# Performance work log

Hardware: AMD Instinct MI355X
Metric: run time of the kernel (lower is better)

Reference implementation:

```python
import jax, jax.numpy as jnp
import numpy as np

PATCH = 8
C1 = 1e-4
C2 = 1e-3
EPS = 1e-3
ALPHA = 0.4
WEIGHTS = (1.0, 0.01, 1.0)


def charbonnier(x):
    return (x * x + EPS * EPS) ** ALPHA


def resize_bilinear_ac(img, H2, W2):
    # bilinear resize with align_corners=True (matches F.interpolate)
    B, C, H, W = img.shape
    fy = jnp.arange(H2, dtype=img.dtype) * ((H - 1) / max(H2 - 1, 1))
    fx = jnp.arange(W2, dtype=img.dtype) * ((W - 1) / max(W2 - 1, 1))
    y0 = jnp.clip(jnp.floor(fy).astype(jnp.int32), 0, H - 2)
    x0 = jnp.clip(jnp.floor(fx).astype(jnp.int32), 0, W - 2)
    wy = (fy - y0)[None, None, :, None]
    wx = (fx - x0)[None, None, None, :]
    rows = img[:, :, y0, :] * (1 - wy) + img[:, :, y0 + 1, :] * wy  # [B,C,H2,W]
    out = rows[:, :, :, x0] * (1 - wx) + rows[:, :, :, x0 + 1] * wx  # [B,C,H2,W2]
    return out


def bilinear_warp(img, flow):
    # backward warp: sample img at (x + u, y + v), bilinear, border clamp
    B, C, H, W = img.shape
    gx = jnp.arange(W, dtype=img.dtype)[None, None, :] + flow[:, 0]  # [B,H,W]
    gy = jnp.arange(H, dtype=img.dtype)[None, :, None] + flow[:, 1]  # [B,H,W]
    x0f = jnp.floor(gx)
    y0f = jnp.floor(gy)
    wx = (gx - x0f)[:, None]  # [B,1,H,W]
    wy = (gy - y0f)[:, None]
    x0 = jnp.clip(x0f.astype(jnp.int32), 0, W - 1)
    x1 = jnp.clip(x0 + 1, 0, W - 1)
    y0 = jnp.clip(y0f.astype(jnp.int32), 0, H - 1)
    y1 = jnp.clip(y0 + 1, 0, H - 1)
    imgf = img.reshape(B, C, H * W)

    def gather(yi, xi):
        idx = (yi * W + xi).reshape(B, 1, H * W)
        g = jnp.take_along_axis(imgf, jnp.broadcast_to(idx, (B, C, H * W)), axis=2)
        return g.reshape(B, C, H, W)

    v00 = gather(y0, x0)
    v01 = gather(y0, x1)
    v10 = gather(y1, x0)
    v11 = gather(y1, x1)
    top = v00 * (1 - wx) + v01 * wx
    bot = v10 * (1 - wx) + v11 * wx
    return top * (1 - wy) + bot * wy


def torch_gradient(x, axis):
    # torch.gradient: central diff interior, one-sided at edges, spacing 1
    n = x.shape[axis]
    sl = lambda a, b: jax.lax.slice_in_dim(x, a, b, axis=axis)
    first = sl(1, 2) - sl(0, 1)
    interior = (sl(2, n) - sl(0, n - 2)) * 0.5
    last = sl(n - 1, n) - sl(n - 2, n - 1)
    return jnp.concatenate([first, interior, last], axis=axis)


def ssim_score(I1, I2):
    # faithful to SSIMLoss: stats pooled over ALL non-overlapping patches per
    # (batch, channel), i.e. over the region cropped to multiples of patch.
    B, C, H, W = I1.shape
    p = min(PATCH, H)
    PH, PW = H // p, W // p
    x = I1[:, :, :PH * p, :PW * p].reshape(B, C, -1)
    y = I2[:, :, :PH * p, :PW * p].reshape(B, C, -1)
    N = x.shape[-1]
    mu1 = x.mean(-1)
    mu2 = y.mean(-1)
    d1 = x - mu1[..., None]
    d2 = y - mu2[..., None]
    var1 = (d1 * d1).sum(-1) / (N - 1)  # torch .var() is unbiased
    var2 = (d2 * d2).sum(-1) / (N - 1)
    s12 = (d1 * d2).mean(-1)
    num = (2 * mu1 * mu2 + C1) * (2 * s12 + C2)
    den = (mu1 ** 2 + mu2 ** 2 + C1) * (var1 + var2 + C2)
    return num / den  # [B, C]


def setup_inputs() -> dict:
    key = jax.random.key(0)
    k1, k2 = jax.random.split(key)
    images = jax.random.uniform(k1, (16, 33, 256, 256), dtype=jnp.float32)
    flows = jax.random.normal(k2, (16, 20, 128, 128), dtype=jnp.float32)
    return {"images": images, "flows": flows}


def reference(images, flows):
    B, Cf, FH, FW = flows.shape
    n_flows = Cf // 2  # 10 frame pairs
    imgs = resize_bilinear_ac(images, FH, FW)  # [B,33,FH,FW]
    src = imgs[:, 3:].reshape(B * n_flows, 3, FH, FW)
    fl = flows.reshape(B * n_flows, 2, FH, FW)
    warped = bilinear_warp(src, fl).reshape(B, n_flows * 3, FH, FW)
    ref = imgs[:, : n_flows * 3]

    similarity_loss = ssim_score(ref, warped).mean()

    flow_x = flows[:, 0::2]
    flow_y = flows[:, 1::2]
    smooth = (charbonnier(torch_gradient(flow_x, 1))
              + charbonnier(torch_gradient(flow_x, 2))
              + charbonnier(torch_gradient(flow_y, 1))
              + charbonnier(torch_gradient(flow_y, 2))).mean()

    pixel_loss = charbonnier(ref - warped).mean()

    return WEIGHTS[0] * pixel_loss + WEIGHTS[1] * smooth + WEIGHTS[2] * similarity_loss
```

## Files before the change

kernel.cpp:

```cpp
#include <hip/hip_runtime.h>

#define IH 256
#define IW 256
#define FH 128
#define FW 128
#define NB 16
#define ICH 33
#define NF 10
#define NC 30
#define PL (FH * FW)
#define ACC_FLOATS 3848
#define RES_OFF 4096
#define RES_CNT (NB * ICH * PL)
#define WS_NEED ((size_t)(RES_OFF + RES_CNT) * 4)

__device__ __forceinline__ float charb(float g) {
    float t = fmaf(g, g, 1e-6f);
    return __builtin_amdgcn_exp2f(0.4f * __builtin_amdgcn_logf(t));
}

__global__ void __launch_bounds__(256) resize_kernel(const float* __restrict__ images,
                                                     float* __restrict__ resized,
                                                     float* __restrict__ acc)
{
    if (blockIdx.x == 0) {
        for (int i = threadIdx.x; i < ACC_FLOATS; i += 256) acc[i] = 0.f;
    }
    __shared__ float rows[4][256];
    const float s = (float)(255.0 / 127.0);
    int plane = blockIdx.x >> 6;
    int j = blockIdx.x & 63;
    int h0 = 2 * j;
    int y0a = (int)((float)h0 * s);       if (y0a > IH - 2) y0a = IH - 2;
    int y0b = (int)((float)(h0 + 1) * s); if (y0b > IH - 2) y0b = IH - 2;
    int rowidx[4] = { y0a, y0a + 1, y0b, y0b + 1 };
    const float* pin = images + (size_t)plane * (IH * IW);
    int r = threadIdx.x >> 6;
    int l = threadIdx.x & 63;
    const float4* srcv = (const float4*)(pin + rowidx[r] * IW);
    ((float4*)rows[r])[l] = srcv[l];
    __syncthreads();
    int lr = threadIdx.x >> 7;
    int w = threadIdx.x & 127;
    int h = h0 + lr;
    float fy = (float)h * s;
    int y0 = lr ? y0b : y0a;
    float wy = fy - (float)y0;
    float fx = (float)w * s;
    int x0 = (int)fx; if (x0 > IW - 2) x0 = IW - 2;
    float wx = fx - (float)x0;
    float v00 = rows[2 * lr][x0],     v01 = rows[2 * lr][x0 + 1];
    float v10 = rows[2 * lr + 1][x0], v11 = rows[2 * lr + 1][x0 + 1];
    float r0 = v00 * (1.f - wy) + v10 * wy;
    float r1 = v01 * (1.f - wy) + v11 * wy;
    resized[(size_t)plane * PL + h * FW + w] = r0 * (1.f - wx) + r1 * wx;
}

__device__ __forceinline__ float warp_sample(const float* __restrict__ src_plane,
                                             float gx, float gy) {
    float x0f = floorf(gx), y0f = floorf(gy);
    float wx = gx - x0f, wy = gy - y0f;
    int x0 = (int)x0f; x0 = min(max(x0, 0), FW - 1);
    int y0 = (int)y0f; y0 = min(max(y0, 0), FH - 1);
    int x1 = min(x0 + 1, FW - 1);
    int y1 = min(y0 + 1, FH - 1);
    const float* r0p = src_plane + y0 * FW;
    const float* r1p = src_plane + y1 * FW;
    float v00 = r0p[x0], v01 = r0p[x1];
    float v10 = r1p[x0], v11 = r1p[x1];
    float top = v00 * (1.f - wx) + v01 * wx;
    float bot = v10 * (1.f - wx) + v11 * wx;
    return top * (1.f - wy) + bot * wy;
}

#define SPLIT 4
#define LOSS_BLOCKS (NB * NC * SPLIT)
#define SMOOTH_BLOCKS 1280
#define PIX_PER_BLOCK (PL / SPLIT)
__global__ void __launch_bounds__(256) fat_kernel(const float* __restrict__ resized,
                                                  const float* __restrict__ flows,
                                                  float* __restrict__ acc_bc,
                                                  float* __restrict__ acc_g)
{
    if (blockIdx.x < LOSS_BLOCKS) {
        int bc = blockIdx.x / SPLIT;
        int part = blockIdx.x % SPLIT;
        int b = bc / NC;
        int c = bc % NC;
        int f = c / 3;
        const float* ref_plane = resized + (size_t)(b * ICH + c) * PL;
        const float* src_plane = resized + (size_t)(b * ICH + 3 + c) * PL;
        const float* fx_plane  = flows + (size_t)(b * 2 * NF + 2 * f) * PL;
        const float* fy_plane  = fx_plane + PL;

        float s_ref = 0.f, s_w = 0.f, s_r2 = 0.f, s_w2 = 0.f, s_rw = 0.f, s_pix = 0.f;
        int base2 = part * (PIX_PER_BLOCK / 2);
        for (int i = threadIdx.x; i < PIX_PER_BLOCK / 2; i += 256) {
            int pix2 = base2 + i;
            int pix = pix2 * 2;
            int h = pix >> 7;
            int w = pix & (FW - 1);
            float2 ref2 = ((const float2*)ref_plane)[pix2];
            float2 fx2  = ((const float2*)fx_plane)[pix2];
            float2 fy2  = ((const float2*)fy_plane)[pix2];

            float wv0 = warp_sample(src_plane, (float)w + fx2.x,       (float)h + fy2.x);
            float wv1 = warp_sample(src_plane, (float)(w + 1) + fx2.y, (float)h + fy2.y);

            s_ref += ref2.x + ref2.y;
            s_w   += wv0 + wv1;
            s_r2  += ref2.x * ref2.x + ref2.y * ref2.y;
            s_w2  += wv0 * wv0 + wv1 * wv1;
            s_rw  += ref2.x * wv0 + ref2.y * wv1;
            s_pix += charb(ref2.x - wv0) + charb(ref2.y - wv1);
        }
        for (int off = 32; off > 0; off >>= 1) {
            s_ref += __shfl_down(s_ref, off, 64);
            s_w   += __shfl_down(s_w, off, 64);
            s_r2  += __shfl_down(s_r2, off, 64);
            s_w2  += __shfl_down(s_w2, off, 64);
            s_rw  += __shfl_down(s_rw, off, 64);
            s_pix += __shfl_down(s_pix, off, 64);
        }
        __shared__ float sh[4][6];
        int wave = threadIdx.x >> 6;
        if ((threadIdx.x & 63) == 0) {
            sh[wave][0] = s_ref; sh[wave][1] = s_w; sh[wave][2] = s_r2;
            sh[wave][3] = s_w2;  sh[wave][4] = s_rw; sh[wave][5] = s_pix;
        }
        __syncthreads();
        if (threadIdx.x == 0) {
            float t0 = 0, t1 = 0, t2 = 0, t3 = 0, t4 = 0, t5 = 0;
            for (int v = 0; v < 4; v++) {
                t0 += sh[v][0]; t1 += sh[v][1]; t2 += sh[v][2];
                t3 += sh[v][3]; t4 += sh[v][4]; t5 += sh[v][5];
            }
            float* a = acc_bc + bc * 8;
            atomicAdd(a + 0, t0);
            atomicAdd(a + 1, t1);
            atomicAdd(a + 2, t2);
            atomicAdd(a + 3, t3);
            atomicAdd(a + 4, t4);
            atomicAdd(acc_g + 0, t5);
        }
    } else {
        const int total = NB * NF * PL;
        float s = 0.f;
        for (int i = (blockIdx.x - LOSS_BLOCKS) * 256 + threadIdx.x; i < total;
             i += SMOOTH_BLOCKS * 256) {
            int w = i & (FW - 1);
            int h = (i >> 7) & (FH - 1);
            int f = (i >> 14) % NF;
            int b = i / (NF * PL);
            int pix = h * FW + w;
            const float* xp = flows + (size_t)(b * 2 * NF + 2 * f) * PL;
            const float* yp = xp + PL;

            float g1x, g1y;
            if (f == 0)           { g1x = xp[2 * PL + pix] - xp[pix];
                                    g1y = yp[2 * PL + pix] - yp[pix]; }
            else if (f == NF - 1) { g1x = xp[pix] - xp[pix - 2 * PL];
                                    g1y = yp[pix] - yp[pix - 2 * PL]; }
            else                  { g1x = 0.5f * (xp[2 * PL + pix] - xp[pix - 2 * PL]);
                                    g1y = 0.5f * (yp[2 * PL + pix] - yp[pix - 2 * PL]); }

            float g2x, g2y;
            if (h == 0)           { g2x = xp[pix + FW] - xp[pix];
                                    g2y = yp[pix + FW] - yp[pix]; }
            else if (h == FH - 1) { g2x = xp[pix] - xp[pix - FW];
                                    g2y = yp[pix] - yp[pix - FW]; }
            else                  { g2x = 0.5f * (xp[pix + FW] - xp[pix - FW]);
                                    g2y = 0.5f * (yp[pix + FW] - yp[pix - FW]); }

            s += charb(g1x) + charb(g2x) + charb(g1y) + charb(g2y);
        }
        for (int off = 32; off > 0; off >>= 1) s += __shfl_down(s, off, 64);
        __shared__ float shs[4];
        int wave = threadIdx.x >> 6;
        if ((threadIdx.x & 63) == 0) shs[wave] = s;
        __syncthreads();
        if (threadIdx.x == 0)
            atomicAdd(acc_g + 2, shs[0] + shs[1] + shs[2] + shs[3]);
    }
}

__global__ void __launch_bounds__(512) finalize(const float* __restrict__ acc_bc,
                                                const float* __restrict__ acc_g,
                                                float* __restrict__ out)
{
    __shared__ float sh[512];
    int tid = threadIdx.x;
    float ssim = 0.f;
    if (tid < NB * NC) {
        const float* a = acc_bc + tid * 8;
        const float N = (float)PL;
        float mu1 = a[0] / N, mu2 = a[1] / N;
        float var1 = (a[2] - a[0] * mu1) / (N - 1.f);
        float var2 = (a[3] - a[1] * mu2) / (N - 1.f);
        float s12 = a[4] / N - mu1 * mu2;
        float num = (2.f * mu1 * mu2 + 1e-4f) * (2.f * s12 + 1e-3f);
        float den = (mu1 * mu1 + mu2 * mu2 + 1e-4f) * (var1 + var2 + 1e-3f);
        ssim = num / den;
    }
    sh[tid] = ssim;
    __syncthreads();
    for (int off = 256; off > 0; off >>= 1) {
        if (tid < off) sh[tid] += sh[tid + off];
        __syncthreads();
    }
    if (tid == 0) {
        float pix    = acc_g[0] / (float)(NB * NC * PL);
        float smooth = acc_g[2] / (float)(NB * NF * PL);
        float sim    = sh[0] / (float)(NB * NC);
        out[0] = pix + 0.01f * smooth + sim;
    }
}

__device__ __forceinline__ float resized_at(const float* __restrict__ plane, int Y, int X) {
    const float s = (float)(255.0 / 127.0);
    float fy = (float)Y * s;
    float fx = (float)X * s;
    int y0 = (int)fy; y0 = y0 > IH - 2 ? IH - 2 : y0;
    int x0 = (int)fx; x0 = x0 > IW - 2 ? IW - 2 : x0;
    float wy = fy - (float)y0;
    float wx = fx - (float)x0;
    const float* p0 = plane + y0 * IW + x0;
    float v00 = p0[0], v01 = p0[1];
    float v10 = p0[IW], v11 = p0[IW + 1];
    float r0 = v00 * (1.f - wy) + v10 * wy;
    float r1 = v01 * (1.f - wy) + v11 * wy;
    return r0 * (1.f - wx) + r1 * wx;
}

__global__ void __launch_bounds__(256) loss_main_fb(const float* __restrict__ images,
                                                    const float* __restrict__ flows,
                                                    float* __restrict__ acc_bc,
                                                    float* __restrict__ acc_g)
{
    int bc = blockIdx.x / 8;
    int part = blockIdx.x % 8;
    int b = bc / NC;
    int c = bc % NC;
    int f = c / 3;
    const float* ref_plane = images + (size_t)(b * ICH + c) * (IH * IW);
    const float* src_plane = images + (size_t)(b * ICH + 3 + c) * (IH * IW);
    const float* fx_plane  = flows + (size_t)(b * 2 * NF + 2 * f) * PL;
    const float* fy_plane  = fx_plane + PL;

    float s_ref = 0.f, s_w = 0.f, s_r2 = 0.f, s_w2 = 0.f, s_rw = 0.f, s_pix = 0.f;
    int base = part * (PL / 8);
    for (int i = threadIdx.x; i < PL / 8; i += 256) {
        int pix = base + i;
        int h = pix >> 7;
        int w = pix & (FW - 1);
        float ref = resized_at(ref_plane, h, w);
        float fxv = fx_plane[pix];
        float fyv = fy_plane[pix];
        float gx = (float)w + fxv;
        float gy = (float)h + fyv;
        float x0f = floorf(gx), y0f = floorf(gy);
        float wx = gx - x0f, wy = gy - y0f;
        int x0 = (int)x0f; x0 = min(max(x0, 0), FW - 1);
        int y0 = (int)y0f; y0 = min(max(y0, 0), FH - 1);
        int x1 = min(x0 + 1, FW - 1);
        int y1 = min(y0 + 1, FH - 1);
        float v00 = resized_at(src_plane, y0, x0);
        float v01 = resized_at(src_plane, y0, x1);
        float v10 = resized_at(src_plane, y1, x0);
        float v11 = resized_at(src_plane, y1, x1);
        float top = v00 * (1.f - wx) + v01 * wx;
        float bot = v10 * (1.f - wx) + v11 * wx;
        float wv = top * (1.f - wy) + bot * wy;
        s_ref += ref; s_w += wv;
        s_r2 += ref * ref; s_w2 += wv * wv; s_rw += ref * wv;
        s_pix += charb(ref - wv);
    }
    for (int off = 32; off > 0; off >>= 1) {
        s_ref += __shfl_down(s_ref, off, 64);
        s_w   += __shfl_down(s_w, off, 64);
        s_r2  += __shfl_down(s_r2, off, 64);
        s_w2  += __shfl_down(s_w2, off, 64);
        s_rw  += __shfl_down(s_rw, off, 64);
        s_pix += __shfl_down(s_pix, off, 64);
    }
    if ((threadIdx.x & 63) == 0) {
        float* a = acc_bc + bc * 8;
        atomicAdd(a + 0, s_ref);
        atomicAdd(a + 1, s_w);
        atomicAdd(a + 2, s_r2);
        atomicAdd(a + 3, s_w2);
        atomicAdd(a + 4, s_rw);
        atomicAdd(acc_g + 0, s_pix);
    }
}

__global__ void __launch_bounds__(256) smooth_fb(const float* __restrict__ flows,
                                                 float* __restrict__ acc_g)
{
    const int total = NB * NF * PL;
    float s = 0.f;
    for (int i = blockIdx.x * 256 + threadIdx.x; i < total; i += 1280 * 256) {
        int w = i & (FW - 1);
        int h = (i >> 7) & (FH - 1);
        int f = (i >> 14) % NF;
        int b = i / (NF * PL);
        int pix = h * FW + w;
        const float* xp = flows + (size_t)(b * 2 * NF + 2 * f) * PL;
        const float* yp = xp + PL;
        float g1x, g1y;
        if (f == 0)           { g1x = xp[2 * PL + pix] - xp[pix];
                                g1y = yp[2 * PL + pix] - yp[pix]; }
        else if (f == NF - 1) { g1x = xp[pix] - xp[pix - 2 * PL];
                                g1y = yp[pix] - yp[pix - 2 * PL]; }
        else                  { g1x = 0.5f * (xp[2 * PL + pix] - xp[pix - 2 * PL]);
                                g1y = 0.5f * (yp[2 * PL + pix] - yp[pix - 2 * PL]); }
        float g2x, g2y;
        if (h == 0)           { g2x = xp[pix + FW] - xp[pix];
                                g2y = yp[pix + FW] - yp[pix]; }
        else if (h == FH - 1) { g2x = xp[pix] - xp[pix - FW];
                                g2y = yp[pix] - yp[pix - FW]; }
        else                  { g2x = 0.5f * (xp[pix + FW] - xp[pix - FW]);
                                g2y = 0.5f * (yp[pix + FW] - yp[pix - FW]); }
        s += charb(g1x) + charb(g2x) + charb(g1y) + charb(g2y);
    }
    for (int off = 32; off > 0; off >>= 1) s += __shfl_down(s, off, 64);
    __shared__ float sh[4];
    int wave = threadIdx.x >> 6;
    if ((threadIdx.x & 63) == 0) sh[wave] = s;
    __syncthreads();
    if (threadIdx.x == 0)
        atomicAdd(acc_g + 2, sh[0] + sh[1] + sh[2] + sh[3]);
}

extern "C" void kernel_launch(void* const* d_in, const int* in_sizes, int n_in,
                              void* d_out, int out_size, void* d_ws, size_t ws_size,
                              hipStream_t stream) {
    const float* images = (const float*)d_in[0];
    const float* flows  = (const float*)d_in[1];
    float* acc_bc  = (float*)d_ws;
    float* acc_g   = acc_bc + NB * NC * 8;
    float* resized = (float*)d_ws + RES_OFF;
    if (ws_size >= WS_NEED) {
        resize_kernel<<<NB * ICH * (FH / 2), 256, 0, stream>>>(images, resized, acc_bc);
        fat_kernel<<<LOSS_BLOCKS + SMOOTH_BLOCKS, 256, 0, stream>>>(resized, flows,
                                                                    acc_bc, acc_g);
    } else {
        (void)hipMemsetAsync(d_ws, 0, ACC_FLOATS * sizeof(float), stream);
        loss_main_fb<<<NB * NC * 8, 256, 0, stream>>>(images, flows, acc_bc, acc_g);
        smooth_fb<<<1280, 256, 0, stream>>>(flows, acc_g);
    }
    finalize<<<1, 512, 0, stream>>>(acc_bc, acc_g, (float*)d_out);
}
```

Before: 261.6 us.

## Move smoothness term into resize kernel and fuse finalize via last-block counter

The flow smoothness reduction moves from the loss kernel into the resize kernel, so it runs alongside the resize and writes per-block partials instead of using atomics. The finalize kernel is removed: the last loss block, found with an atomic counter and a threadfence, computes SSIM and the final sum. The loss kernel now processes four pixels per thread with float4 loads, and its block index is remapped so each batch image's blocks land on one XCD for L2 locality. This saves a kernel launch and the tail of the loss kernel, but adds the threadfence and counter ordering and has the last block re-read the accumulators with atomics.

Result: slower. 285.4 us (+9.1%).

```diff
diff --git a/kernel.cpp b/kernel.cpp
--- a/kernel.cpp
+++ b/kernel.cpp
@@ -9,8 +9,10 @@
 #define NF 10
 #define NC 30
 #define PL (FH * FW)
-#define ACC_FLOATS 3848
-#define RES_OFF 4096
+#define ACC_ZERO 3856
+#define SMOOTH_BLK 1280
+#define RES_BLK (NB * ICH * 64)
+#define RES_OFF 8192
 #define RES_CNT (NB * ICH * PL)
 #define WS_NEED ((size_t)(RES_OFF + RES_CNT) * 4)
 
@@ -19,25 +21,71 @@
     return __builtin_amdgcn_exp2f(0.4f * __builtin_amdgcn_logf(t));
 }
 
-__global__ void __launch_bounds__(256) resize_kernel(const float* __restrict__ images,
-                                                     float* __restrict__ resized,
-                                                     float* __restrict__ acc)
+__global__ void __launch_bounds__(256) k1_smooth_resize(const float* __restrict__ images,
+                                                        const float* __restrict__ flows,
+                                                        float* __restrict__ ws)
 {
+    float* acc         = ws;
+    float* smooth_part = ws + ACC_ZERO;
+    float* resized     = ws + RES_OFF;
+
     if (blockIdx.x == 0) {
-        for (int i = threadIdx.x; i < ACC_FLOATS; i += 256) acc[i] = 0.f;
-    }
+        for (int i = threadIdx.x; i < ACC_ZERO; i += 256) acc[i] = 0.f;
+    }
+
+    if (blockIdx.x < SMOOTH_BLK) {
+        const int total = NB * NF * PL;
+        float s = 0.f;
+        for (int i = blockIdx.x * 256 + threadIdx.x; i < total; i += SMOOTH_BLK * 256) {
+            int w = i & (FW - 1);
+            int h = (i >> 7) & (FH - 1);
+            int f = (i >> 14) % NF;
+            int b = i / (NF * PL);
+            int pix = h * FW + w;
+            const float* xp = flows + (size_t)(b * 2 * NF + 2 * f) * PL;
+            const float* yp = xp + PL;
+
+            float g1x, g1y;
+            if (f == 0)           { g1x = xp[2 * PL + pix] - xp[pix];
+                                    g1y = yp[2 * PL + pix] - yp[pix]; }
+            else if (f == NF - 1) { g1x = xp[pix] - xp[pix - 2 * PL];
+                                    g1y = yp[pix] - yp[pix - 2 * PL]; }
+            else                  { g1x = 0.5f * (xp[2 * PL + pix] - xp[pix - 2 * PL]);
+                                    g1y = 0.5f * (yp[2 * PL + pix] - yp[pix - 2 * PL]); }
+
+            float g2x, g2y;
+            if (h == 0)           { g2x = xp[pix + FW] - xp[pix];
+                                    g2y = yp[pix + FW] - yp[pix]; }
+            else if (h == FH - 1) { g2x = xp[pix] - xp[pix - FW];
+                                    g2y = yp[pix] - yp[pix - FW]; }
+            else                  { g2x = 0.5f * (xp[pix + FW] - xp[pix - FW]);
+                                    g2y = 0.5f * (yp[pix + FW] - yp[pix - FW]); }
+
+            s += charb(g1x) + charb(g2x) + charb(g1y) + charb(g2y);
+        }
+        for (int off = 32; off > 0; off >>= 1) s += __shfl_down(s, off, 64);
+        __shared__ float shs[4];
+        int wave = threadIdx.x >> 6;
+        if ((threadIdx.x & 63) == 0) shs[wave] = s;
+        __syncthreads();
+        if (threadIdx.x == 0)
+            smooth_part[blockIdx.x] = shs[0] + shs[1] + shs[2] + shs[3];
+        return;
+    }
+
+    int rb = blockIdx.x - SMOOTH_BLK;
     __shared__ float rows[4][256];
     const float s = (float)(255.0 / 127.0);
-    int plane = blockIdx.x >> 6;
-    int j = blockIdx.x & 63;
+    int plane = rb >> 6;
+    int j = rb & 63;
     int h0 = 2 * j;
     int y0a = (int)((float)h0 * s);       if (y0a > IH - 2) y0a = IH - 2;
     int y0b = (int)((float)(h0 + 1) * s); if (y0b > IH - 2) y0b = IH - 2;
-    int rowidx[4] = { y0a, y0a + 1, y0b, y0b + 1 };
     const float* pin = images + (size_t)plane * (IH * IW);
     int r = threadIdx.x >> 6;
     int l = threadIdx.x & 63;
-    const float4* srcv = (const float4*)(pin + rowidx[r] * IW);
+    int yr = (r < 2 ? y0a : y0b) + (r & 1);
+    const float4* srcv = (const float4*)(pin + yr * IW);
     ((float4*)rows[r])[l] = srcv[l];
     __syncthreads();
     int lr = threadIdx.x >> 7;
@@ -75,144 +123,128 @@
 
 #define SPLIT 4
 #define LOSS_BLOCKS (NB * NC * SPLIT)
-#define SMOOTH_BLOCKS 1280
 #define PIX_PER_BLOCK (PL / SPLIT)
-__global__ void __launch_bounds__(256) fat_kernel(const float* __restrict__ resized,
-                                                  const float* __restrict__ flows,
-                                                  float* __restrict__ acc_bc,
-                                                  float* __restrict__ acc_g)
+__global__ void __launch_bounds__(256) k2_loss_final(const float* __restrict__ flows,
+                                                     float* __restrict__ ws,
+                                                     float* __restrict__ out)
 {
-    if (blockIdx.x < LOSS_BLOCKS) {
-        int bc = blockIdx.x / SPLIT;
-        int part = blockIdx.x % SPLIT;
-        int b = bc / NC;
-        int c = bc % NC;
-        int f = c / 3;
-        const float* ref_plane = resized + (size_t)(b * ICH + c) * PL;
-        const float* src_plane = resized + (size_t)(b * ICH + 3 + c) * PL;
-        const float* fx_plane  = flows + (size_t)(b * 2 * NF + 2 * f) * PL;
-        const float* fy_plane  = fx_plane + PL;
-
-        float s_ref = 0.f, s_w = 0.f, s_r2 = 0.f, s_w2 = 0.f, s_rw = 0.f, s_pix = 0.f;
-        int base2 = part * (PIX_PER_BLOCK / 2);
-        for (int i = threadIdx.x; i < PIX_PER_BLOCK / 2; i += 256) {
-            int pix2 = base2 + i;
-            int pix = pix2 * 2;
-            int h = pix >> 7;
-            int w = pix & (FW - 1);
-            float2 ref2 = ((const float2*)ref_plane)[pix2];
-            float2 fx2  = ((const float2*)fx_plane)[pix2];
-            float2 fy2  = ((const float2*)fy_plane)[pix2];
-
-            float wv0 = warp_sample(src_plane, (float)w + fx2.x,       (float)h + fy2.x);
-            float wv1 = warp_sample(src_plane, (float)(w + 1) + fx2.y, (float)h + fy2.y);
-
-            s_ref += ref2.x + ref2.y;
-            s_w   += wv0 + wv1;
-            s_r2  += ref2.x * ref2.x + ref2.y * ref2.y;
-            s_w2  += wv0 * wv0 + wv1 * wv1;
-            s_rw  += ref2.x * wv0 + ref2.y * wv1;
-            s_pix += charb(ref2.x - wv0) + charb(ref2.y - wv1);
+    float* acc_bc      = ws;
+    float* acc_g       = ws + 3840;
+    unsigned* counter  = (unsigned*)(ws + 3848);
+    const float* smooth_part = ws + ACC_ZERO;
+    const float* resized     = ws + RES_OFF;
+
+    int xcd  = blockIdx.x & 7;
+    int slot = blockIdx.x >> 3;
+    int hi   = (slot >= 120) ? 1 : 0;
+    int b    = xcd + 8 * hi;
+    int j    = slot - 120 * hi;
+    int c    = j >> 2;
+    int part = j & 3;
+    int bc   = b * NC + c;
+    int f    = c / 3;
+
+    const float* ref_plane = resized + (size_t)(b * ICH + c) * PL;
+    const float* src_plane = resized + (size_t)(b * ICH + 3 + c) * PL;
+    const float* fx_plane  = flows + (size_t)(b * 2 * NF + 2 * f) * PL;
+    const float* fy_plane  = fx_plane + PL;
+
+    float s_ref = 0.f, s_w = 0.f, s_r2 = 0.f, s_w2 = 0.f, s_rw = 0.f, s_pix = 0.f;
+    int base4 = part * (PIX_PER_BLOCK / 4);
+    for (int i = threadIdx.x; i < PIX_PER_BLOCK / 4; i += 256) {
+        int p4 = base4 + i;
+        int pix = p4 * 4;
+        int h = pix >> 7;
+        int w = pix & (FW - 1);
+        float4 r4 = ((const float4*)ref_plane)[p4];
+        float4 fx4 = ((const float4*)fx_plane)[p4];
+        float4 fy4 = ((const float4*)fy_plane)[p4];
+        float fh = (float)h, fw0 = (float)w;
+
+        float wv0 = warp_sample(src_plane, fw0 + fx4.x,       fh + fy4.x);
+        float wv1 = warp_sample(src_plane, fw0 + 1.f + fx4.y, fh + fy4.y);
+        float wv2 = warp_sample(src_plane, fw0 + 2.f + fx4.z, fh + fy4.z);
+        float wv3 = warp_sample(src_plane, fw0 + 3.f + fx4.w, fh + fy4.w);
+
+        s_ref += (r4.x + r4.y) + (r4.z + r4.w);
+        s_w   += (wv0 + wv1) + (wv2 + wv3);
+        s_r2  += r4.x * r4.x + r4.y * r4.y + r4.z * r4.z + r4.w * r4.w;
+        s_w2  += wv0 * wv0 + wv1 * wv1 + wv2 * wv2 + wv3 * wv3;
+        s_rw  += r4.x * wv0 + r4.y * wv1 + r4.z * wv2 + r4.w * wv3;
+        s_pix += charb(r4.x - wv0) + charb(r4.y - wv1)
+               + charb(r4.z - wv2) + charb(r4.w - wv3);
+    }
+    for (int off = 32; off > 0; off >>= 1) {
+        s_ref += __shfl_down(s_ref, off, 64);
+        s_w   += __shfl_down(s_w, off, 64);
+        s_r2  += __shfl_down(s_r2, off, 64);
+        s_w2  += __shfl_down(s_w2, off, 64);
+        s_rw  += __shfl_down(s_rw, off, 64);
+        s_pix += __shfl_down(s_pix, off, 64);
+    }
+    __shared__ float sh[4][6];
+    __shared__ int last_flag;
+    int wave = threadIdx.x >> 6;
+    if ((threadIdx.x & 63) == 0) {
+        sh[wave][0] = s_ref; sh[wave][1] = s_w; sh[wave][2] = s_r2;
+        sh[wave][3] = s_w2;  sh[wave][4] = s_rw; sh[wave][5] = s_pix;
+    }
+    __syncthreads();
+    if (threadIdx.x == 0) {
+        float t0 = 0, t1 = 0, t2 = 0, t3 = 0, t4 = 0, t5 = 0;
+        for (int v = 0; v < 4; v++) {
+            t0 += sh[v][0]; t1 += sh[v][1]; t2 += sh[v][2];
+            t3 += sh[v][3]; t4 += sh[v][4]; t5 += sh[v][5];
         }
-        for (int off = 32; off > 0; off >>= 1) {
-            s_ref += __shfl_down(s_ref, off, 64);
-            s_w   += __shfl_down(s_w, off, 64);
-            s_r2  += __shfl_down(s_r2, off, 64);
-            s_w2  += __shfl_down(s_w2, off, 64);
-            s_rw  += __shfl_down(s_rw, off, 64);
-            s_pix += __shfl_down(s_pix, off, 64);
-        }
-        __shared__ float sh[4][6];
-        int wave = threadIdx.x >> 6;
-        if ((threadIdx.x & 63) == 0) {
-            sh[wave][0] = s_ref; sh[wave][1] = s_w; sh[wave][2] = s_r2;
-            sh[wave][3] = s_w2;  sh[wave][4] = s_rw; sh[wave][5] = s_pix;
-        }
-        __syncthreads();
-        if (threadIdx.x == 0) {
-            float t0 = 0, t1 = 0, t2 = 0, t3 = 0, t4 = 0, t5 = 0;
-            for (int v = 0; v < 4; v++) {
-                t0 += sh[v][0]; t1 += sh[v][1]; t2 += sh[v][2];
-                t3 += sh[v][3]; t4 += sh[v][4]; t5 += sh[v][5];
-            }
-            float* a = acc_bc + bc * 8;
-            atomicAdd(a + 0, t0);
-            atomicAdd(a + 1, t1);
-            atomicAdd(a + 2, t2);
-            atomicAdd(a + 3, t3);
-            atomicAdd(a + 4, t4);
-            atomicAdd(acc_g + 0, t5);
-        }
-    } else {
-        const int total = NB * NF * PL;
-        float s = 0.f;
-        for (int i = (blockIdx.x - LOSS_BLOCKS) * 256 + threadIdx.x; i < total;
-             i += SMOOTH_BLOCKS * 256) {
-            int w = i & (FW - 1);
-            int h = (i >> 7) & (FH - 1);
-            int f = (i >> 14) % NF;
-            int b = i / (NF * PL);
-            int pix = h * FW + w;
-            const float* xp = flows + (size_t)(b * 2 * NF + 2 * f) * PL;
-            const float* yp = xp + PL;
-
-            float g1x, g1y;
-            if (f == 0)           { g1x = xp[2 * PL + pix] - xp[pix];
-                                    g1y = yp[2 * PL + pix] - yp[pix]; }
-            else if (f == NF - 1) { g1x = xp[pix] - xp[pix - 2 * PL];
-                                    g1y = yp[pix] - yp[pix - 2 * PL]; }
-            else                  { g1x = 0.5f * (xp[2 * PL + pix] - xp[pix - 2 * PL]);
-                                    g1y = 0.5f * (yp[2 * PL + pix] - yp[pix - 2 * PL]); }
-
-            float g2x, g2y;
-            if (h == 0)           { g2x = xp[pix + FW] - xp[pix];
-                                    g2y = yp[pix + FW] - yp[pix]; }
-            else if (h == FH - 1) { g2x = xp[pix] - xp[pix - FW];
-                                    g2y = yp[pix] - yp[pix - FW]; }
-            else                  { g2x = 0.5f * (xp[pix + FW] - xp[pix - FW]);
-                                    g2y = 0.5f * (yp[pix + FW] - yp[pix - FW]); }
-
-            s += charb(g1x) + charb(g2x) + charb(g1y) + charb(g2y);
-        }
-        for (int off = 32; off > 0; off >>= 1) s += __shfl_down(s, off, 64);
-        __shared__ float shs[4];
-        int wave = threadIdx.x >> 6;
-        if ((threadIdx.x & 63) == 0) shs[wave] = s;
-        __syncthreads();
-        if (threadIdx.x == 0)
-            atomicAdd(acc_g + 2, shs[0] + shs[1] + shs[2] + shs[3]);
-    }
-}
-
-__global__ void __launch_bounds__(512) finalize(const float* __restrict__ acc_bc,
-                                                const float* __restrict__ acc_g,
-                                                float* __restrict__ out)
-{
-    __shared__ float sh[512];
-    int tid = threadIdx.x;
-    float ssim = 0.f;
-    if (tid < NB * NC) {
-        const float* a = acc_bc + tid * 8;
+        float* a = acc_bc + bc * 8;
+        atomicAdd(a + 0, t0);
+        atomicAdd(a + 1, t1);
+        atomicAdd(a + 2, t2);
+        atomicAdd(a + 3, t3);
+        atomicAdd(a + 4, t4);
+        atomicAdd(acc_g + 0, t5);
+        __threadfence();
+        unsigned old = atomicAdd(counter, 1u);
+        last_flag = (old == LOSS_BLOCKS - 1) ? 1 : 0;
+    }
+    __syncthreads();
+    if (!last_flag) return;
+
+    float ssim_s = 0.f;
+    for (int e = threadIdx.x; e < NB * NC; e += 256) {
+        float* a = acc_bc + e * 8;
+        float t0 = atomicAdd(a + 0, 0.f);
+        float t1 = atomicAdd(a + 1, 0.f);
+        float t2 = atomicAdd(a + 2, 0.f);
+        float t3 = atomicAdd(a + 3, 0.f);
+        float t4 = atomicAdd(a + 4, 0.f);
         const float N = (float)PL;
-        float mu1 = a[0] / N, mu2 = a[1] / N;
-        float var1 = (a[2] - a[0] * mu1) / (N - 1.f);
-        float var2 = (a[3] - a[1] * mu2) / (N - 1.f);
-        float s12 = a[4] / N - mu1 * mu2;
+        float mu1 = t0 / N, mu2 = t1 / N;
+        float var1 = (t2 - t0 * mu1) / (N - 1.f);
+        float var2 = (t3 - t1 * mu2) / (N - 1.f);
+        float s12 = t4 / N - mu1 * mu2;
         float num = (2.f * mu1 * mu2 + 1e-4f) * (2.f * s12 + 1e-3f);
         float den = (mu1 * mu1 + mu2 * mu2 + 1e-4f) * (var1 + var2 + 1e-3f);
-        ssim = num / den;
-    }
-    sh[tid] = ssim;
-    __syncthreads();
-    for (int off = 256; off > 0; off >>= 1) {
-        if (tid < off) sh[tid] += sh[tid + off];
-        __syncthreads();
-    }
-    if (tid == 0) {
-        float pix    = acc_g[0] / (float)(NB * NC * PL);
-        float smooth = acc_g[2] / (float)(NB * NF * PL);
-        float sim    = sh[0] / (float)(NB * NC);
-        out[0] = pix + 0.01f * smooth + sim;
+        ssim_s += num / den;
+    }
+    float smooth_s = 0.f;
+    for (int i = threadIdx.x; i < SMOOTH_BLK; i += 256)
+        smooth_s += smooth_part[i];
+
+    for (int off = 32; off > 0; off >>= 1) {
+        ssim_s   += __shfl_down(ssim_s, off, 64);
+        smooth_s += __shfl_down(smooth_s, off, 64);
+    }
+    __shared__ float fs[4][2];
+    if ((threadIdx.x & 63) == 0) { fs[wave][0] = ssim_s; fs[wave][1] = smooth_s; }
+    __syncthreads();
+    if (threadIdx.x == 0) {
+        float ssim_t = fs[0][0] + fs[1][0] + fs[2][0] + fs[3][0];
+        float smo_t  = fs[0][1] + fs[1][1] + fs[2][1] + fs[3][1];
+        float pix_t  = atomicAdd(acc_g + 0, 0.f);
+        out[0] = pix_t / (float)(NB * NC * PL)
+               + 0.01f * (smo_t / (float)(NB * NF * PL))
+               + ssim_t / (float)(NB * NC);
     }
 }
 
@@ -246,7 +278,6 @@
     const float* src_plane = images + (size_t)(b * ICH + 3 + c) * (IH * IW);
     const float* fx_plane  = flows + (size_t)(b * 2 * NF + 2 * f) * PL;
     const float* fy_plane  = fx_plane + PL;
-
     float s_ref = 0.f, s_w = 0.f, s_r2 = 0.f, s_w2 = 0.f, s_rw = 0.f, s_pix = 0.f;
     int base = part * (PL / 8);
     for (int i = threadIdx.x; i < PL / 8; i += 256) {
@@ -254,10 +285,8 @@
         int h = pix >> 7;
         int w = pix & (FW - 1);
         float ref = resized_at(ref_plane, h, w);
-        float fxv = fx_plane[pix];
-        float fyv = fy_plane[pix];
-        float gx = (float)w + fxv;
-        float gy = (float)h + fyv;
+        float gx = (float)w + fx_plane[pix];
+        float gy = (float)h + fy_plane[pix];
         float x0f = floorf(gx), y0f = floorf(gy);
         float wx = gx - x0f, wy = gy - y0f;
         int x0 = (int)x0f; x0 = min(max(x0, 0), FW - 1);
@@ -332,22 +361,52 @@
         atomicAdd(acc_g + 2, sh[0] + sh[1] + sh[2] + sh[3]);
 }
 
+__global__ void __launch_bounds__(512) finalize_fb(const float* __restrict__ acc_bc,
+                                                   const float* __restrict__ acc_g,
+                                                   float* __restrict__ out)
+{
+    __shared__ float sh[512];
+    int tid = threadIdx.x;
+    float ssim = 0.f;
+    if (tid < NB * NC) {
+        const float* a = acc_bc + tid * 8;
+        const float N = (float)PL;
+        float mu1 = a[0] / N, mu2 = a[1] / N;
+        float var1 = (a[2] - a[0] * mu1) / (N - 1.f);
+        float var2 = (a[3] - a[1] * mu2) / (N - 1.f);
+        float s12 = a[4] / N - mu1 * mu2;
+        float num = (2.f * mu1 * mu2 + 1e-4f) * (2.f * s12 + 1e-3f);
+        float den = (mu1 * mu1 + mu2 * mu2 + 1e-4f) * (var1 + var2 + 1e-3f);
+        ssim = num / den;
+    }
+    sh[tid] = ssim;
+    __syncthreads();
+    for (int off = 256; off > 0; off >>= 1) {
+        if (tid < off) sh[tid] += sh[tid + off];
+        __syncthreads();
+    }
+    if (tid == 0) {
+        out[0] = acc_g[0] / (float)(NB * NC * PL)
+               + 0.01f * (acc_g[2] / (float)(NB * NF * PL))
+               + sh[0] / (float)(NB * NC);
+    }
+}
+
 extern "C" void kernel_launch(void* const* d_in, const int* in_sizes, int n_in,
                               void* d_out, int out_size, void* d_ws, size_t ws_size,
                               hipStream_t stream) {
     const float* images = (const float*)d_in[0];
     const float* flows  = (const float*)d_in[1];
-    float* acc_bc  = (float*)d_ws;
-    float* acc_g   = acc_bc + NB * NC * 8;
-    float* resized = (float*)d_ws + RES_OFF;
+    float* ws = (float*)d_ws;
     if (ws_size >= WS_NEED) {
-        resize_kernel<<<NB * ICH * (FH / 2), 256, 0, stream>>>(images, resized, acc_bc);
-        fat_kernel<<<LOSS_BLOCKS + SMOOTH_BLOCKS, 256, 0, stream>>>(resized, flows,
-                                                                    acc_bc, acc_g);
+        k1_smooth_resize<<<SMOOTH_BLK + RES_BLK, 256, 0, stream>>>(images, flows, ws);
+        k2_loss_final<<<LOSS_BLOCKS, 256, 0, stream>>>(flows, ws, (float*)d_out);
     } else {
-        (void)hipMemsetAsync(d_ws, 0, ACC_FLOATS * sizeof(float), stream);
+        float* acc_bc = ws;
+        float* acc_g  = ws + 3840;
+        (void)hipMemsetAsync(d_ws, 0, ACC_ZERO * sizeof(float), stream);
         loss_main_fb<<<NB * NC * 8, 256, 0, stream>>>(images, flows, acc_bc, acc_g);
         smooth_fb<<<1280, 256, 0, stream>>>(flows, acc_g);
-    }
-    finalize<<<1, 512, 0, stream>>>(acc_bc, acc_g, (float*)d_out);
-}
+        finalize_fb<<<1, 512, 0, stream>>>(acc_bc, acc_g, (float*)d_out);
+    }
+}
```
